# Optimization experiments

Measured on AMD Instinct MI355X. Metric: run time of the kernel, lower is better.

The kernel has to match this reference:

```python
import jax, jax.numpy as jnp
import numpy as np

KH = KW = 3
SH = SW = 1
PH = PW = 1


def _im2col(x, kh, kw, sh, sw, ph, pw):
    # x: [N, C, H, W] -> cols: [N, C*kh*kw, H_out*W_out], ordering (C, kh, kw)
    N, C, H, W = x.shape
    H_out = (H + 2 * ph - kh) // sh + 1
    W_out = (W + 2 * pw - kw) // sw + 1
    x_pad = jnp.pad(x, ((0, 0), (0, 0), (ph, ph), (pw, pw)))
    # fixed small loop over kernel offsets (kh*kw = 9), strided slices
    patches = [x_pad[:, :, i:i + sh * H_out:sh, j:j + sw * W_out:sw]
               for i in range(kh) for j in range(kw)]  # each [N, C, H_out, W_out]
    cols = jnp.stack(patches, axis=2)  # [N, C, kh*kw, H_out, W_out]
    cols = cols.reshape(N, C * kh * kw, H_out * W_out)
    return cols, H_out, W_out


def setup_inputs() -> dict:
    key = jax.random.key(0)
    k1, k2, k3 = jax.random.split(key, 3)
    x = jax.random.normal(k1, (16, 128, 56, 56), dtype=jnp.float32)
    weight = jax.random.normal(k2, (256, 128, 3, 3), dtype=jnp.float32) * 0.05
    fan_in = 128 * 3 * 3
    bound = 1.0 / fan_in ** 0.5
    bias = jax.random.uniform(k3, (256,), dtype=jnp.float32, minval=-bound, maxval=bound)
    return {"x": x, "weight": weight, "bias": bias}


def reference(x, weight, bias):
    # im2col unfold + (analog) matmul conv; noise_cfg=None -> plain matmul
    cols, H_out, W_out = _im2col(x, KH, KW, SH, SW, PH, PW)  # [N, K, L]
    N = cols.shape[0]
    Cout = weight.shape[0]
    Wmat = weight.reshape(Cout, -1)  # [Cout, K], K = C*kh*kw
    # y[n, l, o] = sum_k cols[n, k, l] * Wmat[o, k]  (AnalogMatMulFn without noise)
    y = jnp.einsum('nkl,ok->nol', cols, Wmat)  # [N, Cout, L]
    y = y.reshape(N, Cout, H_out, W_out)
    y = y + bias[None, :, None, None]
    return y
```

## Files before the change

### kernel.cpp

```cpp
#include <hip/hip_runtime.h>
#include <hip/hip_bf16.h>
#include <stdint.h>


typedef __attribute__((ext_vector_type(8))) short short8;
typedef __attribute__((ext_vector_type(4))) float floatx4;

__device__ static inline void gload_lds16(const void* g, void* l) {
  typedef const __attribute__((address_space(1))) unsigned int* gp_t;
  typedef __attribute__((address_space(3))) unsigned int* lp_t;
  __builtin_amdgcn_global_load_lds((gp_t)(uintptr_t)g, (lp_t)(uint32_t)(uintptr_t)l,
                                   16, 0, 0);
}

__global__ __launch_bounds__(256)
void pre_kernel(const float* __restrict__ x, const float* __restrict__ wsrc,
                __hip_bfloat16* __restrict__ xp, __hip_bfloat16* __restrict__ wt) {
  const int b = blockIdx.x;
  if (b < 16 * 58) {
    const int n = b / 58, hp = b % 58;
    __hip_bfloat16* dst = xp + (size_t)(n * 58 + hp) * 58 * 128;
    if (hp == 0 || hp == 57) {
      const uint4 z = {0, 0, 0, 0};
      uint4* p = (uint4*)dst;
      for (int i = threadIdx.x; i < 928; i += 256) p[i] = z;
      return;
    }
    const int h = hp - 1;
    __shared__ float tile[128][57];
    const float* src = x + (size_t)n * (128 * 3136) + h * 56;
    for (int i = threadIdx.x; i < 128 * 14; i += 256) {
      const int c = i / 14, q = i - c * 14;
      const float4 v = ((const float4*)(src + (size_t)c * 3136))[q];
      tile[c][4 * q + 0] = v.x;
      tile[c][4 * q + 1] = v.y;
      tile[c][4 * q + 2] = v.z;
      tile[c][4 * q + 3] = v.w;
    }
    __syncthreads();
    if (threadIdx.x < 32) {
      const uint4 z = {0, 0, 0, 0};
      const int col = (threadIdx.x >> 4) * 57;
      ((uint4*)(dst + (size_t)col * 128))[threadIdx.x & 15] = z;
    }
    __hip_bfloat16* di = dst + 128;
    for (int i = threadIdx.x; i < 56 * 16; i += 256) {
      const int w = i >> 4, c8 = (i & 15) * 8;
      union { uint4 u; __hip_bfloat16 hh[8]; } pk;
#pragma unroll
      for (int j = 0; j < 8; ++j) pk.hh[j] = __float2bfloat16(tile[c8 + j][w]);
      *(uint4*)(di + (size_t)w * 128 + c8) = pk.u;
    }
  } else {
    const int base = (b - 928) * 256 + threadIdx.x;
    for (int t = base; t < 256 * 9 * 128; t += 36 * 256) {
      const int e = t & 7;
      const int rr = (t >> 3) & 15;
      const int q = (t >> 7) & 3;
      const int ks = (t >> 9) & 1;
      const int ch = (t >> 10) & 1;
      const int t11 = t >> 11;
      const int kq = t11 % 9;
      const int g = t11 / 9;
      const int cout = g * 16 + rr;
      const int c = ch * 64 + ks * 32 + q * 8 + e;
      wt[t] = __float2bfloat16(wsrc[(size_t)(cout * 128 + c) * 9 + kq]);
    }
  }
}

__global__ __launch_bounds__(256, 3)
void conv_gemm_kernel(const __hip_bfloat16* __restrict__ xp,
                      const __hip_bfloat16* __restrict__ wt,
                      const float* __restrict__ bias,
                      float* __restrict__ out) {
  __shared__ __align__(16) char smem[49152];

  const int tid = threadIdx.x;
  const int lane = tid & 63;
  const int wave = tid >> 6;
  const int col = lane & 15;
  const int quad = lane >> 4;

  const int id = blockIdx.x;
  const int xcd = id & 7;
  const int nt_ = xcd * 98 + (id >> 3);
  const int n0 = nt_ * 64;

  const int nimg0 = n0 / 3136;
  const int rem0 = n0 - nimg0 * 3136;
  const int hh0 = rem0 / 56;
  const int ww0 = rem0 - hh0 * 56;
  const int P0 = (nimg0 * 58 + hh0) * 58 + ww0;
  const char* pbase = (const char*)xp + (size_t)P0 * 256;

#pragma unroll
  for (int i = 0; i < 12; ++i) {
    const int j = i * 256 + tid;
    const int row = j >> 4;
    const int slot = j & 15;
    gload_lds16(pbase + row * 256 + ((slot ^ (row & 7)) << 4),
                smem + i * 4096 + wave * 1024);
  }

  const char* wtb = (const char*)wt;
  const char* pA[4];
#pragma unroll
  for (int mt = 0; mt < 4; ++mt)
    pA[mt] = wtb + (size_t)(wave * 4 + mt) * 36864 + lane * 16;

  short8 areg[2][4];
#pragma unroll
  for (int mt = 0; mt < 4; ++mt) areg[0][mt] = *(const short8*)(pA[mt]);

  int rbase[4];
#pragma unroll
  for (int nt = 0; nt < 4; ++nt) {
    const int pix = n0 + nt * 16 + col;
    const int ni = pix / 3136;
    const int re = pix - ni * 3136;
    const int ph = re / 56;
    const int pw = re - ph * 56;
    rbase[nt] = (ni * 58 + ph) * 58 + pw - P0;
  }

  floatx4 acc[4][4];
#pragma unroll
  for (int a = 0; a < 4; ++a)
#pragma unroll
    for (int c = 0; c < 4; ++c) acc[a][c] = (floatx4)0.f;

  __syncthreads();

  short8 bfr[2][4];
#pragma unroll
  for (int nt = 0; nt < 4; ++nt) {
    const int rowB = rbase[nt];
    const int pos = quad ^ (rowB & 7);
    bfr[0][nt] = *(const short8*)(smem + rowB * 256 + (pos << 4));
  }

#pragma unroll
  for (int s = 0; s < 36; ++s) {
    if (s < 35) {
      const int s1 = s + 1;
      const int kq1 = s1 >> 2;
      const int ksl = s1 & 3;
      const int nb = s1 & 1;
      const int ofs = kq1 * 4096 + ksl * 1024;
#pragma unroll
      for (int mt = 0; mt < 4; ++mt)
        areg[nb][mt] = *(const short8*)(pA[mt] + ofs);
      const int kh1 = kq1 / 3;
      const int tofs1 = kh1 * 58 + (kq1 - kh1 * 3);
#pragma unroll
      for (int nt = 0; nt < 4; ++nt) {
        const int rowB = rbase[nt] + tofs1;
        const int cB = ksl * 4 + quad;
        const int pos = cB ^ (rowB & 7);
        bfr[nb][nt] = *(const short8*)(smem + rowB * 256 + (pos << 4));
      }
    }
    const int cb = s & 1;
#pragma unroll
    for (int mt = 0; mt < 4; ++mt)
#pragma unroll
      for (int nt = 0; nt < 4; ++nt)
        acc[mt][nt] = __builtin_amdgcn_mfma_f32_16x16x32_bf16(
            areg[cb][mt], bfr[cb][nt], acc[mt][nt], 0, 0, 0);
  }

  const int rb = quad * 4;
#pragma unroll
  for (int nt = 0; nt < 4; ++nt) {
    const int pix = n0 + nt * 16 + col;
    const int nimg = pix / 3136;
    const int rem = pix - nimg * 3136;
    float* op = out + (size_t)nimg * (256 * 3136) + rem;
#pragma unroll
    for (int mt = 0; mt < 4; ++mt) {
      const int mb = wave * 64 + mt * 16 + rb;
#pragma unroll
      for (int rr = 0; rr < 4; ++rr) {
        op[(size_t)(mb + rr) * 3136] = acc[mt][nt][rr] + bias[mb + rr];
      }
    }
  }
}

__global__ __launch_bounds__(256)
void direct_conv_kernel(const float* __restrict__ x, const float* __restrict__ wgt,
                        const float* __restrict__ bias, float* __restrict__ out) {
  const long t = (long)blockIdx.x * 256 + threadIdx.x;
  if (t >= 16L * 256 * 3136) return;
  const int w = t % 56;
  const int h = (t / 56) % 56;
  const int o = (t / 3136) % 256;
  const int n = t / (256L * 3136);
  float s = bias[o];
  for (int c = 0; c < 128; ++c)
    for (int kh = 0; kh < 3; ++kh) {
      const int hh = h + kh - 1;
      if (hh < 0 || hh >= 56) continue;
      for (int kw = 0; kw < 3; ++kw) {
        const int ww = w + kw - 1;
        if (ww < 0 || ww >= 56) continue;
        s += x[((size_t)(n * 128 + c) * 56 + hh) * 56 + ww] *
             wgt[((size_t)(o * 128 + c) * 3 + kh) * 3 + kw];
      }
    }
  out[t] = s;
}

extern "C" void kernel_launch(void* const* d_in, const int* in_sizes, int n_in,
                              void* d_out, int out_size, void* d_ws, size_t ws_size,
                              hipStream_t stream) {
  const float* x = (const float*)d_in[0];
  const float* w = (const float*)d_in[1];
  const float* b = (const float*)d_in[2];
  float* out = (float*)d_out;

  const size_t xp_bytes = (size_t)16 * 58 * 58 * 128 * 2;
  const size_t wt_bytes = (size_t)256 * 9 * 128 * 2;

  if (ws_size >= xp_bytes + wt_bytes) {
    __hip_bfloat16* xp = (__hip_bfloat16*)d_ws;
    __hip_bfloat16* wt = (__hip_bfloat16*)((char*)d_ws + xp_bytes);
    hipLaunchKernelGGL(pre_kernel, dim3(16 * 58 + 36), dim3(256), 0, stream,
                       x, w, xp, wt);
    hipLaunchKernelGGL(conv_gemm_kernel, dim3(784), dim3(256), 0, stream,
                       xp, wt, b, out);
  } else {
    const long total = 16L * 256 * 3136;
    hipLaunchKernelGGL(direct_conv_kernel, dim3((unsigned)((total + 255) / 256)),
                       dim3(256), 0, stream, x, w, b, out);
  }
}
```

Measured before the change: 141.2 us.

## Double-buffer input rows per kernel-height tap to overlap loads and cut LDS

The conv GEMM kernel no longer loads the whole 48KB padded input window into LDS up front. It now stages one kernel-row slab (about 17KB) at a time into two alternating buffers and overlaps the next slab's global-to-LDS load with MFMA compute on the current one. The smaller LDS footprint allows occupancy to rise from 3 to 4 blocks per CU. The explicit register double-buffering of A/B fragments is dropped in favor of simple per-step loads, which risks exposing load latency if the compiler schedules poorly.

Result: slower. 183.4 us (+29.9%).

```diff
diff --git a/kernel.cpp b/kernel.cpp
--- a/kernel.cpp
+++ b/kernel.cpp
@@ -69,12 +69,12 @@
   }
 }
 
-__global__ __launch_bounds__(256, 3)
+__global__ __launch_bounds__(256, 4)
 void conv_gemm_kernel(const __hip_bfloat16* __restrict__ xp,
                       const __hip_bfloat16* __restrict__ wt,
                       const float* __restrict__ bias,
                       float* __restrict__ out) {
-  __shared__ __align__(16) char smem[49152];
+  __shared__ __align__(16) char smem[2][17408];
 
   const int tid = threadIdx.x;
   const int lane = tid & 63;
@@ -94,24 +94,31 @@
   const int P0 = (nimg0 * 58 + hh0) * 58 + ww0;
   const char* pbase = (const char*)xp + (size_t)P0 * 256;
 
-#pragma unroll
-  for (int i = 0; i < 12; ++i) {
-    const int j = i * 256 + tid;
-    const int row = j >> 4;
-    const int slot = j & 15;
-    gload_lds16(pbase + row * 256 + ((slot ^ (row & 7)) << 4),
-                smem + i * 4096 + wave * 1024);
-  }
+  auto stage = [&](int ph, char* buf) {
+    const char* src = pbase + ph * (58 * 256);
+#pragma unroll
+    for (int i = 0; i < 4; ++i) {
+      const int j = i * 256 + tid;
+      const int row = j >> 4;
+      const int slot = j & 15;
+      gload_lds16(src + row * 256 + ((slot ^ (row & 7)) << 4),
+                  buf + i * 4096 + wave * 1024);
+    }
+    if (wave == 0) {
+      const int j = 1024 + lane;
+      const int row = j >> 4;
+      const int slot = j & 15;
+      gload_lds16(src + row * 256 + ((slot ^ (row & 7)) << 4), buf + 16384);
+    }
+  };
+
+  stage(0, smem[0]);
 
   const char* wtb = (const char*)wt;
   const char* pA[4];
 #pragma unroll
   for (int mt = 0; mt < 4; ++mt)
     pA[mt] = wtb + (size_t)(wave * 4 + mt) * 36864 + lane * 16;
-
-  short8 areg[2][4];
-#pragma unroll
-  for (int mt = 0; mt < 4; ++mt) areg[0][mt] = *(const short8*)(pA[mt]);
 
   int rbase[4];
 #pragma unroll
@@ -130,45 +137,40 @@
 #pragma unroll
     for (int c = 0; c < 4; ++c) acc[a][c] = (floatx4)0.f;
 
+  short8 areg[4], bfr[4];
+
+  auto compute = [&](int p, const char* buf) {
+#pragma unroll
+    for (int t = 0; t < 12; ++t) {
+      const int kw = t >> 2;
+      const int ksl = t & 3;
+      const int ofs = (p * 3 + kw) * 4096 + ksl * 1024;
+#pragma unroll
+      for (int mt = 0; mt < 4; ++mt)
+        areg[mt] = *(const short8*)(pA[mt] + ofs);
+#pragma unroll
+      for (int nt = 0; nt < 4; ++nt) {
+        const int rowL = rbase[nt] + kw;
+        const int pos = (ksl * 4 + quad) ^ (rowL & 7);
+        bfr[nt] = *(const short8*)(buf + rowL * 256 + (pos << 4));
+      }
+#pragma unroll
+      for (int mt = 0; mt < 4; ++mt)
+#pragma unroll
+        for (int nt = 0; nt < 4; ++nt)
+          acc[mt][nt] = __builtin_amdgcn_mfma_f32_16x16x32_bf16(
+              areg[mt], bfr[nt], acc[mt][nt], 0, 0, 0);
+    }
+  };
+
   __syncthreads();
-
-  short8 bfr[2][4];
-#pragma unroll
-  for (int nt = 0; nt < 4; ++nt) {
-    const int rowB = rbase[nt];
-    const int pos = quad ^ (rowB & 7);
-    bfr[0][nt] = *(const short8*)(smem + rowB * 256 + (pos << 4));
-  }
-
-#pragma unroll
-  for (int s = 0; s < 36; ++s) {
-    if (s < 35) {
-      const int s1 = s + 1;
-      const int kq1 = s1 >> 2;
-      const int ksl = s1 & 3;
-      const int nb = s1 & 1;
-      const int ofs = kq1 * 4096 + ksl * 1024;
-#pragma unroll
-      for (int mt = 0; mt < 4; ++mt)
-        areg[nb][mt] = *(const short8*)(pA[mt] + ofs);
-      const int kh1 = kq1 / 3;
-      const int tofs1 = kh1 * 58 + (kq1 - kh1 * 3);
-#pragma unroll
-      for (int nt = 0; nt < 4; ++nt) {
-        const int rowB = rbase[nt] + tofs1;
-        const int cB = ksl * 4 + quad;
-        const int pos = cB ^ (rowB & 7);
-        bfr[nb][nt] = *(const short8*)(smem + rowB * 256 + (pos << 4));
-      }
-    }
-    const int cb = s & 1;
-#pragma unroll
-    for (int mt = 0; mt < 4; ++mt)
-#pragma unroll
-      for (int nt = 0; nt < 4; ++nt)
-        acc[mt][nt] = __builtin_amdgcn_mfma_f32_16x16x32_bf16(
-            areg[cb][mt], bfr[cb][nt], acc[mt][nt], 0, 0, 0);
-  }
+  stage(1, smem[1]);
+  compute(0, smem[0]);
+  __syncthreads();
+  stage(2, smem[0]);
+  compute(1, smem[1]);
+  __syncthreads();
+  compute(2, smem[0]);
 
   const int rb = quad * 4;
 #pragma unroll
```
